# Kernel optimization log

Measured on AMD Instinct MI355X. Metric: run time of the kernel, lower is better.

## Reference

```python
import jax, jax.numpy as jnp
import numpy as np
from itertools import permutations, combinations

BATCH = 32768
EPS = 1e-06  # positivity eps from __init__


def _levi_civita7():
    e = np.zeros((7,) * 7, dtype=np.float32)
    for p in permutations(range(7)):
        inv = sum(1 for i in range(7) for j in range(i + 1, 7) if p[i] > p[j])
        e[p] = -1.0 if inv % 2 else 1.0
    return jnp.asarray(e)

_EPS7 = _levi_civita7()  # (7,7,7,7,7,7,7) rank-7 Levi-Civita tensor
_TRIPLES = np.array(list(combinations(range(7), 3)), dtype=np.int32)  # (35,3) i<j<k index triples
_PERMS3 = [((0, 1, 2), 1.0), ((1, 2, 0), 1.0), ((2, 0, 1), 1.0),
           ((0, 2, 1), -1.0), ((2, 1, 0), -1.0), ((1, 0, 2), -1.0)]


def _phi_full(phi):
    # expand 35 independent components to fully antisymmetric (B,7,7,7)
    b = phi.shape[0]
    pf = jnp.zeros((b, 7, 7, 7), phi.dtype)
    for perm, s in _PERMS3:
        ia = _TRIPLES[:, perm[0]]
        ib = _TRIPLES[:, perm[1]]
        ic = _TRIPLES[:, perm[2]]
        pf = pf.at[:, ia, ib, ic].set(s * phi)
    return pf


def _metric_from_phi(phi):
    # Standard G2 metric: B_ij = (1/144) phi_ikl phi_jmn phi_pqr eps^{klmnpqr};
    # g = B / |det B|^{1/9}  (unit-determinant normalization)
    pf = _phi_full(phi)  # (B,7,7,7)
    C = jnp.einsum('klmnpqr,bpqr->bklmn', _EPS7, pf)  # (B,7,7,7,7)
    T = jnp.einsum('bklmn,bjmn->bklj', C, pf)          # (B,7,7,7)
    Bm = jnp.einsum('bikl,bklj->bij', pf, T) / 144.0   # (B,7,7)
    det = jnp.linalg.det(Bm)
    g = Bm / (jnp.abs(det)[:, None, None] + 1e-12) ** (1.0 / 9.0)
    return 0.5 * (g + jnp.swapaxes(g, -1, -2))  # exact symmetry for eigvalsh


def setup_inputs() -> dict:
    key = jax.random.key(0)
    phi = jax.random.normal(key, (BATCH, 35), dtype=jnp.float32)
    return {"phi": phi}


def reference(phi):
    g = _metric_from_phi(phi)              # (B,7,7)
    ev = jnp.linalg.eigvalsh(g)            # (B,7)
    return jax.nn.relu(-ev + EPS).sum(axis=-1)  # (B,) sum of negative-eigenvalue violations
```

## Files before the change

kernel.cpp:

```cpp
#include <hip/hip_runtime.h>
#include <utility>

#define BATCH 32768
#define NPHI 35

constexpr int choose2(int n){ return (n*(n-1))/2; }

constexpr int tri_id_sorted(int a,int b,int c){
  int id=0;
  for(int x=0;x<a;++x) id += choose2(6-x);
  for(int y=a+1;y<b;++y) id += (6-y);
  id += (c-b-1);
  return id;
}

constexpr int tri_id3(int a,int b,int c){
  int x=a,y=b,z=c;
  if (x>y){int t=x;x=y;y=t;}
  if (y>z){int t=y;y=z;z=t;}
  if (x>y){int t=x;x=y;y=t;}
  return tri_id_sorted(x,y,z);
}

constexpr int sgn3(int a,int b,int c){
  int inv = (a>b)+(a>c)+(b>c);
  return (inv&1)? -1 : 1;
}

constexpr int UT(int i,int j){
  return i*7 - (i*(i-1))/2 + (j-i);
}

constexpr int PAIR(int k,int l){
  return k*7 - (k*(k+1))/2 + (l - k - 1);
}

struct Prog {
  int n;
  unsigned char kind[1472];
  unsigned char init[1472];
  short         dst [1472];
  unsigned char a   [1472];
  short         b   [1472];
  signed char   s   [1472];
};

constexpr Prog build_prog(){
  Prog P{}; P.n=0;
  bool uinit[28]={};
  for(int k=0;k<7;++k) for(int l=k+1;l<7;++l){
    const int kl = PAIR(k,l);
    bool tinit[7]={};
    for(int m=0;m<7;++m) for(int n2=m+1;n2<7;++n2){
      if(m==k||m==l||n2==k||n2==l) continue;
      int comp[3]={0,0,0}; int cn=0;
      for(int x=0;x<7;++x) if(x!=k&&x!=l&&x!=m&&x!=n2){ comp[cn]=x; ++cn; }
      int perm[7]={k,l,m,n2,comp[0],comp[1],comp[2]};
      int invc=0;
      for(int i=0;i<7;++i) for(int j=i+1;j<7;++j) if(perm[i]>perm[j]) ++invc;
      const int es=(invc&1)? -1 : 1;
      const int tcomp=tri_id_sorted(comp[0],comp[1],comp[2]);
      for(int j=0;j<7;++j){
        if(j==m||j==n2) continue;
        P.kind[P.n]=0;
        P.init[P.n]=tinit[j]?0:1; tinit[j]=true;
        P.dst [P.n]=(short)(kl*7+j);
        P.a   [P.n]=(unsigned char)tcomp;
        P.b   [P.n]=(short)tri_id3(j,m,n2);
        P.s   [P.n]=(signed char)(es*sgn3(j,m,n2));
        ++P.n;
      }
    }
    for(int i=0;i<7;++i){
      if(i==k||i==l) continue;
      for(int j=i;j<7;++j){
        P.kind[P.n]=1;
        P.init[P.n]=uinit[UT(i,j)]?0:1; uinit[UT(i,j)]=true;
        P.dst [P.n]=(short)UT(i,j);
        P.a   [P.n]=(unsigned char)tri_id3(i,k,l);
        P.b   [P.n]=(short)(kl*7+j);
        P.s   [P.n]=(signed char)sgn3(i,k,l);
        ++P.n;
      }
    }
  }
  return P;
}

static constexpr Prog PROG = build_prog();
static_assert(PROG.n == 1470, "program size unexpected");

template<int Q>
__device__ __forceinline__ void step(float (&T)[147], float (&U)[28],
                                     const float (&ph)[NPHI]){
  constexpr int  d = PROG.dst[Q];
  constexpr int  a = PROG.a[Q];
  constexpr int  b = PROG.b[Q];
  constexpr bool neg  = (PROG.s[Q] < 0);
  constexpr bool init = (PROG.init[Q] != 0);
  if constexpr (PROG.kind[Q] == 0){
    const float x = neg ? -ph[a] : ph[a];
    if constexpr (init) T[d] = x * ph[b];
    else                T[d] = fmaf(x, ph[b], T[d]);
  } else {
    const float x = neg ? -ph[a] : ph[a];
    if constexpr (init) U[d] = x * T[b];
    else                U[d] = fmaf(x, T[b], U[d]);
  }
}

template<int... Q>
__device__ __forceinline__ void run_prog(float (&T)[147], float (&U)[28],
                                         const float (&ph)[NPHI],
                                         std::integer_sequence<int, Q...>){
  (step<Q>(T, U, ph), ...);
}

__global__ __launch_bounds__(64,1)
void PositivityConstraint_89086211654295_kernel(const float* __restrict__ phi,
                                                float* __restrict__ out){
  const int gid = blockIdx.x*64 + threadIdx.x;

  const float* __restrict__ p = phi + (size_t)gid * NPHI;
  float ph[NPHI];
  #pragma unroll
  for (int i=0;i<NPHI;++i) ph[i] = p[i];

  float T[147];
  float U[28];
  run_prog(T, U, ph, std::make_integer_sequence<int, PROG.n>{});

  float A[28];
  #pragma unroll
  for (int i=0;i<28;++i) A[i] = U[i]*(1.0f/6.0f);

  for (int sweep=0; sweep<6; ++sweep){
    #pragma unroll
    for (int p1=0;p1<7;++p1){
      #pragma unroll
      for (int q1=p1+1;q1<7;++q1){
        const float apq = A[UT(p1,q1)];
        const float app = A[UT(p1,p1)];
        const float aqq = A[UT(q1,q1)];
        float d = 2.0f*apq;
        d = d + ((d >= 0.0f)? 1e-30f : -1e-30f);
        const float tau = (aqq - app) * __builtin_amdgcn_rcpf(d);
        float t = __builtin_amdgcn_rcpf(
                    fabsf(tau) + __builtin_amdgcn_sqrtf(fmaf(tau,tau,1.0f)));
        t = (tau >= 0.0f)? t : -t;
        const float c = __builtin_amdgcn_rsqf(fmaf(t,t,1.0f));
        const float s = t*c;
        A[UT(p1,p1)] = fmaf(-t, apq, app);
        A[UT(q1,q1)] = fmaf( t, apq, aqq);
        A[UT(p1,q1)] = 0.0f;
        #pragma unroll
        for (int r=0;r<7;++r){
          if (r==p1 || r==q1) continue;
          const int irp = (r<p1)? UT(r,p1) : UT(p1,r);
          const int irq = (r<q1)? UT(r,q1) : UT(q1,r);
          const float arp = A[irp], arq = A[irq];
          A[irp] = fmaf(c, arp, -s*arq);
          A[irq] = fmaf(s, arp,  c*arq);
        }
      }
    }
  }

  float det = 1.0f;
  #pragma unroll
  for (int i=0;i<7;++i) det *= A[UT(i,i)];
  const float ad = fabsf(det) + 1e-12f;
  const float scale = __builtin_amdgcn_exp2f(__builtin_amdgcn_logf(ad) * (1.0f/9.0f));
  const float inv = __builtin_amdgcn_rcpf(scale);

  float sum = 0.0f;
  #pragma unroll
  for (int i=0;i<7;++i){
    const float ev = A[UT(i,i)]*inv;
    const float r = 1e-6f - ev;
    sum += fmaxf(r, 0.0f);
  }
  out[gid] = sum;
}

extern "C" void kernel_launch(void* const* d_in, const int* in_sizes, int n_in,
                              void* d_out, int out_size, void* d_ws, size_t ws_size,
                              hipStream_t stream) {
  const float* phi = (const float*)d_in[0];
  float* out = (float*)d_out;
  (void)in_sizes; (void)n_in; (void)out_size; (void)d_ws; (void)ws_size;
  hipLaunchKernelGGL(PositivityConstraint_89086211654295_kernel,
                     dim3(BATCH/64), dim3(64), 0, stream, phi, out);
}
```

Measured before the change: 65.02 us.

## Use round-robin parallel Jacobi ordering with batched rotation-angle computation

Replaces the cyclic-by-row Jacobi pair order with a round-robin schedule of 7 rounds, each holding 3 disjoint pivot pairs. All three rotations in a round get their angles computed before any is applied, which exposes instruction-level parallelism in place of a serial dependency chain. The angle formula is rewritten to a half-angle form built on rsq/sqrt with no reciprocal of the off-diagonal. The sweep loop is also left un-unrolled to reduce code size. Convergence per sweep may differ slightly from the cyclic order, and the new angle formula changes the numerics.

```diff
diff --git a/kernel.cpp b/kernel.cpp
--- a/kernel.cpp
+++ b/kernel.cpp
@@ -116,6 +116,16 @@
   (step<Q>(T, U, ph), ...);
 }
 
+constexpr int RP[7][3][2] = {
+  {{1,6},{2,5},{3,4}},
+  {{0,1},{2,6},{3,5}},
+  {{0,2},{3,6},{4,5}},
+  {{0,3},{1,2},{4,6}},
+  {{0,4},{1,3},{5,6}},
+  {{0,5},{1,4},{2,3}},
+  {{0,6},{1,5},{2,4}},
+};
+
 __global__ __launch_bounds__(64,1)
 void PositivityConstraint_89086211654295_kernel(const float* __restrict__ phi,
                                                 float* __restrict__ out){
@@ -134,33 +144,46 @@
   #pragma unroll
   for (int i=0;i<28;++i) A[i] = U[i]*(1.0f/6.0f);
 
+  #pragma unroll 1
   for (int sweep=0; sweep<6; ++sweep){
     #pragma unroll
-    for (int p1=0;p1<7;++p1){
+    for (int rr=0; rr<7; ++rr){
+      float c3[3], s3[3], m3[3], av3[3];
       #pragma unroll
-      for (int q1=p1+1;q1<7;++q1){
-        const float apq = A[UT(p1,q1)];
-        const float app = A[UT(p1,p1)];
-        const float aqq = A[UT(q1,q1)];
-        float d = 2.0f*apq;
-        d = d + ((d >= 0.0f)? 1e-30f : -1e-30f);
-        const float tau = (aqq - app) * __builtin_amdgcn_rcpf(d);
-        float t = __builtin_amdgcn_rcpf(
-                    fabsf(tau) + __builtin_amdgcn_sqrtf(fmaf(tau,tau,1.0f)));
-        t = (tau >= 0.0f)? t : -t;
-        const float c = __builtin_amdgcn_rsqf(fmaf(t,t,1.0f));
-        const float s = t*c;
-        A[UT(p1,p1)] = fmaf(-t, apq, app);
-        A[UT(q1,q1)] = fmaf( t, apq, aqq);
+      for (int kp=0; kp<3; ++kp){
+        const int p1 = RP[rr][kp][0], q1 = RP[rr][kp][1];
+        const float app = A[UT(p1,p1)], aqq = A[UT(q1,q1)], apq = A[UT(p1,q1)];
+        const float x   = app - aqq;
+        const float y   = apq + apq;
+        const float ax  = fabsf(x) + 1e-18f;
+        const float ss  = fmaf(ax, ax, y*y);
+        const float w   = __builtin_amdgcn_rsqf(ss);
+        const float u   = ax * w;
+        const float c   = __builtin_amdgcn_sqrtf(fmaf(0.5f, u, 0.5f));
+        const float ss2 = ss + ss;
+        const float dd2 = fmaf(ss2, u, ss2);
+        const float sm  = fabsf(y) * __builtin_amdgcn_rsqf(dd2);
+        const unsigned sb = (__float_as_uint(x) ^ __float_as_uint(y)) & 0x80000000u;
+        const float s1  = sb ? sm : -sm;
+        const float cs  = c * s1;
+        const float m1  = fmaf(0.5f*u, x, -(cs*y));
+        c3[kp]=c; s3[kp]=s1; m3[kp]=m1; av3[kp]=0.5f*(app+aqq);
+      }
+      #pragma unroll
+      for (int kp=0; kp<3; ++kp){
+        const int p1 = RP[rr][kp][0], q1 = RP[rr][kp][1];
+        const float c = c3[kp], s1 = s3[kp];
+        A[UT(p1,p1)] = av3[kp] + m3[kp];
+        A[UT(q1,q1)] = av3[kp] - m3[kp];
         A[UT(p1,q1)] = 0.0f;
         #pragma unroll
-        for (int r=0;r<7;++r){
-          if (r==p1 || r==q1) continue;
-          const int irp = (r<p1)? UT(r,p1) : UT(p1,r);
-          const int irq = (r<q1)? UT(r,q1) : UT(q1,r);
+        for (int r2=0; r2<7; ++r2){
+          if (r2==p1 || r2==q1) continue;
+          const int irp = (r2<p1)? UT(r2,p1) : UT(p1,r2);
+          const int irq = (r2<q1)? UT(r2,q1) : UT(q1,r2);
           const float arp = A[irp], arq = A[irq];
-          A[irp] = fmaf(c, arp, -s*arq);
-          A[irq] = fmaf(s, arp,  c*arq);
+          A[irp] = fmaf(c,  arp, -(s1*arq));
+          A[irq] = fmaf(s1, arp,   c*arq);
         }
       }
     }
```

Result: slower. 67.47 us (+3.8%).
